# Optimization experiments

Measured on AMD Instinct MI355X. Metric: run time of the kernel, lower is better.

The kernel has to match this reference:

```python
import jax, jax.numpy as jnp
import numpy as np

N_NODE = 20000
N_EDGE = 200000
EMBED = 256
PAIR = 128
HEADS = 16
HEAD_DIM = EMBED // HEADS
SCALING = HEAD_DIM ** -0.5
EPS = 1e-5


def _ln(x, w, b):
    m = x.mean(-1, keepdims=True)
    v = ((x - m) ** 2).mean(-1, keepdims=True)
    return (x - m) / jnp.sqrt(v + EPS) * w + b


def setup_inputs() -> dict:
    key = jax.random.key(0)
    ks = jax.random.split(key, 12)
    inp = {
        "query": jax.random.normal(ks[0], (N_NODE, EMBED), jnp.float32),
        "edge_index": jax.random.randint(ks[1], (N_EDGE, 2), 0, N_NODE, jnp.int64 if jax.config.jax_enable_x64 else jnp.int32),
        "edge_diff": jax.random.normal(ks[2], (N_EDGE, 3), jnp.float32),
        "pair": jax.random.normal(ks[3], (N_EDGE, PAIR), jnp.float32),
        "ln_w": jnp.ones((EMBED,), jnp.float32),
        "ln_b": jnp.zeros((EMBED,), jnp.float32),
        "pln_w": jnp.ones((PAIR,), jnp.float32),
        "pln_b": jnp.zeros((PAIR,), jnp.float32),
        "Wq": jax.random.normal(ks[4], (EMBED, EMBED), jnp.float32) * 0.02,
        "Wk": jax.random.normal(ks[5], (EMBED, EMBED), jnp.float32) * 0.02,
        "Wv": jax.random.normal(ks[6], (EMBED, EMBED), jnp.float32) * 0.02,
        "Wb": jax.random.normal(ks[7], (HEADS, PAIR), jnp.float32) * 0.02,
        "bb": jnp.zeros((HEADS,), jnp.float32),
        "Wf1": jax.random.normal(ks[8], (1, EMBED), jnp.float32) * 0.02,
        "bf1": jnp.zeros((1,), jnp.float32),
        "Wf2": jax.random.normal(ks[9], (1, EMBED), jnp.float32) * 0.02,
        "bf2": jnp.zeros((1,), jnp.float32),
        "Wf3": jax.random.normal(ks[10], (1, EMBED), jnp.float32) * 0.02,
        "bf3": jnp.zeros((1,), jnp.float32),
    }
    return inp


def reference(query, edge_index, edge_diff, pair, ln_w, ln_b, pln_w, pln_b,
              Wq, Wk, Wv, Wb, bb, Wf1, bf1, Wf2, bf2, Wf3, bf3):
    n_node = query.shape[0]
    src = edge_index[:, 0]
    dst = edge_index[:, 1]

    qn = _ln(query, ln_w, ln_b)          # preln on node features
    pn = _ln(pair, pln_w, pln_b)         # preln on pair features

    q = (qn @ Wq.T).reshape(n_node, HEADS, HEAD_DIM)
    k = (qn @ Wk.T).reshape(n_node, HEADS, HEAD_DIM)
    v = (qn @ Wv.T).reshape(n_node, HEADS, HEAD_DIM)

    qe = q[src] * SCALING                # [E,H,D]
    ke = k[dst]
    ve = v[dst]

    logits = (qe * ke).sum(-1) + pn @ Wb.T + bb   # [E,H]

    # segment softmax over destination node (edge_index[:,0])
    seg_max = jax.ops.segment_max(logits, src, num_segments=n_node)  # [N,H]
    ex = jnp.exp(logits - seg_max[src])
    denom = jax.ops.segment_sum(ex, src, num_segments=n_node)
    probs = ex / denom[src]              # [E,H]

    # 3D-weighted scatter-sum: out[n,h,c,d] = sum_e probs[e,h]*diff[e,c]*v[e,h,d]
    w = probs[:, :, None] * edge_diff[:, None, :]                    # [E,H,3]
    contrib = w[:, :, :, None] * ve[:, :, None, :]                   # [E,H,3,D]
    x = jax.ops.segment_sum(contrib, src, num_segments=n_node)       # [N,H,3,D]
    x = x.transpose(0, 2, 1, 3).reshape(n_node, 3, EMBED)            # [N,3,H*D]

    f1 = x[:, 0, :] @ Wf1.T + bf1
    f2 = x[:, 1, :] @ Wf2.T + bf2
    f3 = x[:, 2, :] @ Wf3.T + bf3
    return jnp.concatenate([f1, f2, f3], axis=-1).astype(jnp.float32)
```

## Files before the change

### kernel.cpp

```cpp
#include <hip/hip_runtime.h>
#include <math.h>

#define N_NODE 20000
#define N_EDGE 200000
#define EMBED 256
#define PAIR 128
#define HEADS 16
#define HEAD_DIM 16
#define SCALING 0.25f
#define LNEPS 1e-5f

typedef unsigned short u16;
typedef unsigned int u32;
typedef __attribute__((ext_vector_type(8))) short bf16x8;
typedef __attribute__((ext_vector_type(4))) float f32x4;

#define WS_QKV   0
#define WS_QN    30720000
#define WS_WBF   40960000
#define WS_WW    41353216
#define WS_C0    41357312
#define WS_C1    41357376
#define WS_BIAS  41357440
#define WS_VW    54157440
#define WS_CNT   57997440
#define WS_CUR   58077440
#define WS_OFF   58157440
#define WS_REC   58237504

__device__ __forceinline__ u16 f2bf(float f) {
  u32 u = __float_as_uint(f);
  u32 r = (u + 0x7FFFu + ((u >> 16) & 1u)) >> 16;
  return (u16)r;
}
__device__ __forceinline__ float bl(u32 u) { return __uint_as_float(u << 16); }
__device__ __forceinline__ float bh(u32 u) { return __uint_as_float(u & 0xFFFF0000u); }

__device__ __forceinline__ float dot8(uint4 a, uint4 b) {
  float s = bl(a.x) * bl(b.x) + bh(a.x) * bh(b.x);
  s += bl(a.y) * bl(b.y) + bh(a.y) * bh(b.y);
  s += bl(a.z) * bl(b.z) + bh(a.z) * bh(b.z);
  s += bl(a.w) * bl(b.w) + bh(a.w) * bh(b.w);
  return s;
}

__global__ __launch_bounds__(256) void k1_pre_hist_kernel(
    const float* __restrict__ query, const float* __restrict__ ln_w,
    const float* __restrict__ ln_b, u16* __restrict__ qn,
    const float* __restrict__ Wq, const float* __restrict__ Wk,
    const float* __restrict__ Wv, u16* __restrict__ Wbf,
    const float* __restrict__ pln_w, const float* __restrict__ pln_b,
    const float* __restrict__ Wb, const float* __restrict__ bb,
    u16* __restrict__ WWbf, float* __restrict__ c0, float* __restrict__ c1,
    const int* __restrict__ edge_index, int* __restrict__ counts) {
  int bid = blockIdx.x;
  if (bid < 5000) {
    int node = bid * 4 + (threadIdx.x >> 6);
    int lane = threadIdx.x & 63;
    float4 a = *(const float4*)(query + (size_t)node * EMBED + lane * 4);
    float s = a.x + a.y + a.z + a.w;
    float s2 = a.x * a.x + a.y * a.y + a.z * a.z + a.w * a.w;
    #pragma unroll
    for (int off = 32; off > 0; off >>= 1) {
      s += __shfl_xor(s, off);
      s2 += __shfl_xor(s2, off);
    }
    float m = s * (1.0f / EMBED);
    float r = rsqrtf(s2 * (1.0f / EMBED) - m * m + LNEPS);
    float4 w4 = *(const float4*)(ln_w + lane * 4);
    float4 b4 = *(const float4*)(ln_b + lane * 4);
    ushort4 st;
    st.x = f2bf((a.x - m) * r * w4.x + b4.x);
    st.y = f2bf((a.y - m) * r * w4.y + b4.y);
    st.z = f2bf((a.z - m) * r * w4.z + b4.z);
    st.w = f2bf((a.w - m) * r * w4.w + b4.w);
    *(ushort4*)(qn + (size_t)node * EMBED + lane * 4) = st;
  } else if (bid < 5192) {
    int g4 = (bid - 5000) * 256 + threadIdx.x;
    int idx = g4 * 4;
    const float* src = (idx < 65536) ? Wq : (idx < 131072 ? Wk : Wv);
    float4 v = *(const float4*)(src + (idx & 65535));
    ushort4 st = {f2bf(v.x), f2bf(v.y), f2bf(v.z), f2bf(v.w)};
    *(ushort4*)(Wbf + idx) = st;
  } else if (bid == 5192) {
    if (threadIdx.x < 64) {
      int l = threadIdx.x;
      for (int h = 0; h < HEADS; h++) {
        int i0 = l * 2;
        float wb0 = Wb[h * PAIR + i0], wb1 = Wb[h * PAIR + i0 + 1];
        float ww0 = pln_w[i0] * wb0, ww1 = pln_w[i0 + 1] * wb1;
        WWbf[h * PAIR + i0] = f2bf(ww0);
        WWbf[h * PAIR + i0 + 1] = f2bf(ww1);
        float s1 = ww0 + ww1;
        float s0 = pln_b[i0] * wb0 + pln_b[i0 + 1] * wb1;
        #pragma unroll
        for (int off = 32; off > 0; off >>= 1) {
          s1 += __shfl_xor(s1, off);
          s0 += __shfl_xor(s0, off);
        }
        if (l == 0) {
          c1[h] = s1;
          c0[h] = s0 + bb[h];
        }
      }
    }
  } else {
    int e = (bid - 5193) * 256 + threadIdx.x;
    if (e < N_EDGE) atomicAdd(&counts[edge_index[e * 2]], 1);
  }
}

#define BKP 72
__global__ __launch_bounds__(256, 2) void k2_gemm_scan_kernel(
    const u16* __restrict__ qn, const u16* __restrict__ Wbf,
    u16* __restrict__ qkv, const int* __restrict__ counts,
    int* __restrict__ off) {
  int bid = blockIdx.x;
  int t = threadIdx.x;
  if (bid == 942) {
    __shared__ int part[256];
    int i0 = t * 79;
    int i1 = i0 + 79; if (i1 > N_NODE) i1 = N_NODE;
    int s = 0;
    for (int i = i0; i < i1; i++) s += counts[i];
    part[t] = s;
    __syncthreads();
    int x = s;
    for (int o = 1; o < 256; o <<= 1) {
      int y = (t >= o) ? part[t - o] : 0;
      __syncthreads();
      x += y;
      part[t] = x;
      __syncthreads();
    }
    int run = x - s;
    for (int i = i0; i < i1; i++) {
      off[i] = run;
      run += counts[i];
    }
    if (t == 255) off[N_NODE] = N_EDGE;
    return;
  }
  __shared__ u16 As[128 * BKP];
  __shared__ u16 Bs[128 * BKP];
  int bx = bid % 157, by = bid / 157;
  int wv = t >> 6, lane = t & 63;
  int quad = lane >> 4, l16 = lane & 15;
  int row0 = bx * 128, col0 = by * 128;
  int mt = (wv >> 1) * 64, nt = (wv & 1) * 64;

  f32x4 acc[4][4];
  #pragma unroll
  for (int im = 0; im < 4; im++)
    #pragma unroll
    for (int in_ = 0; in_ < 4; in_++) acc[im][in_] = (f32x4){0.f, 0.f, 0.f, 0.f};

  for (int it = 0; it < 4; it++) {
    int k0 = it * 64;
    #pragma unroll
    for (int j = 0; j < 4; j++) {
      int L = j * 256 + t;
      int row = L >> 3, slot = L & 7;
      int ra = min(row0 + row, N_NODE - 1);
      uint4 va = *(const uint4*)(qn + (size_t)ra * 256 + k0 + slot * 8);
      *(uint4*)(&As[row * BKP + slot * 8]) = va;
      uint4 vb = *(const uint4*)(Wbf + (size_t)(col0 + row) * 256 + k0 + slot * 8);
      *(uint4*)(&Bs[row * BKP + slot * 8]) = vb;
    }
    __syncthreads();
    #pragma unroll
    for (int s = 0; s < 2; s++) {
      int ko = s * 32 + quad * 8;
      bf16x8 af[4], bf[4];
      #pragma unroll
      for (int im = 0; im < 4; im++)
        af[im] = *(const bf16x8*)(&As[(mt + im * 16 + l16) * BKP + ko]);
      #pragma unroll
      for (int in_ = 0; in_ < 4; in_++)
        bf[in_] = *(const bf16x8*)(&Bs[(nt + in_ * 16 + l16) * BKP + ko]);
      #pragma unroll
      for (int im = 0; im < 4; im++)
        #pragma unroll
        for (int in_ = 0; in_ < 4; in_++)
          acc[im][in_] = __builtin_amdgcn_mfma_f32_16x16x32_bf16(
              af[im], bf[in_], acc[im][in_], 0, 0, 0);
    }
    __syncthreads();
  }
  #pragma unroll
  for (int im = 0; im < 4; im++) {
    #pragma unroll
    for (int in_ = 0; in_ < 4; in_++) {
      int gcol = col0 + nt + in_ * 16 + l16;
      float scale = (gcol < 256) ? SCALING : 1.0f;
      #pragma unroll
      for (int r = 0; r < 4; r++) {
        int grow = row0 + mt + im * 16 + quad * 4 + r;
        if (grow < N_NODE)
          qkv[(size_t)grow * 768 + gcol] = f2bf(acc[im][in_][r] * scale);
      }
    }
  }
}

#define PP 136
__global__ __launch_bounds__(256) void k3_bias_scatter_vw_kernel(
    const float* __restrict__ pair, const u16* __restrict__ WWbf,
    const float* __restrict__ c0g, const float* __restrict__ c1g,
    float* __restrict__ bias, const u16* __restrict__ qkv,
    const float* __restrict__ Wf1, const float* __restrict__ Wf2,
    const float* __restrict__ Wf3, float* __restrict__ vw,
    const int* __restrict__ edge_index, const float* __restrict__ edge_diff,
    const int* __restrict__ off, int* __restrict__ cur,
    uint4* __restrict__ rec) {
  int bid = blockIdx.x;
  int t = threadIdx.x;
  if (bid >= 3125) {
    int gid = (bid - 3125) * 256 + t;
    int n = gid >> 4, h = gid & 15;
    const uint4* vp = (const uint4*)(qkv + (size_t)n * 768 + 512 + h * 16);
    uint4 va = vp[0], vb = vp[1];
    float v[16];
    v[0] = bl(va.x); v[1] = bh(va.x); v[2] = bl(va.y); v[3] = bh(va.y);
    v[4] = bl(va.z); v[5] = bh(va.z); v[6] = bl(va.w); v[7] = bh(va.w);
    v[8] = bl(vb.x); v[9] = bh(vb.x); v[10] = bl(vb.y); v[11] = bh(vb.y);
    v[12] = bl(vb.z); v[13] = bh(vb.z); v[14] = bl(vb.w); v[15] = bh(vb.w);
    const float* wf[3] = {Wf1 + h * 16, Wf2 + h * 16, Wf3 + h * 16};
    #pragma unroll
    for (int c = 0; c < 3; c++) {
      float s = 0.f;
      #pragma unroll
      for (int d = 0; d < 16; d++) s += v[d] * wf[c][d];
      vw[(size_t)n * 48 + h * 3 + c] = s;
    }
    return;
  }
  __shared__ u16 Ps[64 * PP];
  __shared__ u16 WWs[16 * PP];
  __shared__ float ms[64], rs[64], c0s[16], c1s[16];
  __shared__ int pos_s[64];
  int wv = t >> 6, lane = t & 63;
  int quad = lane >> 4, l16 = lane & 15;
  int e0 = bid * 64;
  #pragma unroll
  for (int j = 0; j < 8; j++) {
    int L = j * 256 + t;
    int row = L >> 5, slot = L & 31;
    float4 p = *(const float4*)(pair + (size_t)(e0 + row) * PAIR + slot * 4);
    ushort4 st = {f2bf(p.x), f2bf(p.y), f2bf(p.z), f2bf(p.w)};
    *(ushort4*)(&Ps[row * PP + slot * 4]) = st;
  }
  #pragma unroll
  for (int j = 0; j < 2; j++) {
    int L = j * 256 + t;
    int row = L >> 5, slot = L & 31;
    ushort4 w = *(const ushort4*)(WWbf + row * PAIR + slot * 4);
    *(ushort4*)(&WWs[row * PP + slot * 4]) = w;
  }
  if (t < 16) {
    c0s[t] = c0g[t];
    c1s[t] = c1g[t];
  }
  if (t < 64) {
    int e = e0 + t;
    int srcn = edge_index[e * 2 + 0];
    int dstn = edge_index[e * 2 + 1];
    int pos = off[srcn] + atomicAdd(&cur[srcn], 1);
    pos_s[t] = pos;
    const float* dp = edge_diff + (size_t)e * 3;
    uint4 r;
    r.x = (u32)dstn;
    r.y = __float_as_uint(dp[0]);
    r.z = __float_as_uint(dp[1]);
    r.w = __float_as_uint(dp[2]);
    rec[pos] = r;
  }
  __syncthreads();
  {
    int row = t >> 2, qq = t & 3;
    float s = 0.f, s2 = 0.f;
    #pragma unroll
    for (int jj = 0; jj < 8; jj++) {
      ushort4 u = *(const ushort4*)(&Ps[row * PP + (qq * 8 + jj) * 4]);
      float x0 = __uint_as_float((u32)u.x << 16);
      float x1 = __uint_as_float((u32)u.y << 16);
      float x2 = __uint_as_float((u32)u.z << 16);
      float x3 = __uint_as_float((u32)u.w << 16);
      s += x0 + x1 + x2 + x3;
      s2 += x0 * x0 + x1 * x1 + x2 * x2 + x3 * x3;
    }
    s += __shfl_xor(s, 1); s += __shfl_xor(s, 2);
    s2 += __shfl_xor(s2, 1); s2 += __shfl_xor(s2, 2);
    if (qq == 0) {
      float m = s * (1.0f / PAIR);
      ms[row] = m;
      rs[row] = rsqrtf(s2 * (1.0f / PAIR) - m * m + LNEPS);
    }
  }
  __syncthreads();
  f32x4 acc = (f32x4){0.f, 0.f, 0.f, 0.f};
  #pragma unroll
  for (int sk = 0; sk < 4; sk++) {
    int ko = sk * 32 + quad * 8;
    bf16x8 a = *(const bf16x8*)(&Ps[(wv * 16 + l16) * PP + ko]);
    bf16x8 b = *(const bf16x8*)(&WWs[l16 * PP + ko]);
    acc = __builtin_amdgcn_mfma_f32_16x16x32_bf16(a, b, acc, 0, 0, 0);
  }
  #pragma unroll
  for (int r = 0; r < 4; r++) {
    int el = wv * 16 + quad * 4 + r;
    float bv = rs[el] * (acc[r] - ms[el] * c1s[l16]) + c0s[l16];
    bias[(size_t)pos_s[el] * HEADS + l16] = bv;
  }
}

__global__ __launch_bounds__(256) void seg_attn_kernel(
    const u16* __restrict__ qkv, const float* __restrict__ bias,
    const int* __restrict__ off, const uint4* __restrict__ rec,
    const float* __restrict__ vw, const float* __restrict__ bf1,
    const float* __restrict__ bf2, const float* __restrict__ bf3,
    float* __restrict__ out) {
  int wv = threadIdx.x >> 6, lane = threadIdx.x & 63;
  int src = blockIdx.x * 4 + wv;
  int h = lane & 15, eslot = lane >> 4;
  int lo = off[src];
  int deg = off[src + 1] - lo;
  const uint4* qp = (const uint4*)(qkv + (size_t)src * 768 + h * 16);
  uint4 q0 = qp[0], q1 = qp[1];
  float exsum = 0.f, a0 = 0.f, a1 = 0.f, a2 = 0.f;
  for (int ei = eslot; ei < deg; ei += 4) {
    uint4 rr = rec[lo + ei];
    int dst = (int)rr.x;
    float d0 = __uint_as_float(rr.y);
    float d1 = __uint_as_float(rr.z);
    float d2 = __uint_as_float(rr.w);
    const uint4* kp = (const uint4*)(qkv + (size_t)dst * 768 + 256 + h * 16);
    float d = dot8(q0, kp[0]) + dot8(q1, kp[1]);
    float ex = __expf(d + bias[(size_t)(lo + ei) * HEADS + h]);
    exsum += ex;
    const float* vp = vw + (size_t)dst * 48 + h * 3;
    a0 += ex * vp[0] * d0;
    a1 += ex * vp[1] * d1;
    a2 += ex * vp[2] * d2;
  }
  exsum += __shfl_xor(exsum, 16);
  exsum += __shfl_xor(exsum, 32);
  float rden = (exsum > 0.f) ? 1.0f / exsum : 0.f;
  a0 *= rden; a1 *= rden; a2 *= rden;
  #pragma unroll
  for (int o = 1; o < 64; o <<= 1) {
    a0 += __shfl_xor(a0, o);
    a1 += __shfl_xor(a1, o);
    a2 += __shfl_xor(a2, o);
  }
  if (lane == 0) {
    out[src * 3 + 0] = a0 + bf1[0];
    out[src * 3 + 1] = a1 + bf2[0];
    out[src * 3 + 2] = a2 + bf3[0];
  }
}

extern "C" void kernel_launch(void* const* d_in, const int* in_sizes, int n_in,
                              void* d_out, int out_size, void* d_ws,
                              size_t ws_size, hipStream_t stream) {
  const float* query      = (const float*)d_in[0];
  const int*   edge_index = (const int*)d_in[1];
  const float* edge_diff  = (const float*)d_in[2];
  const float* pair       = (const float*)d_in[3];
  const float* ln_w       = (const float*)d_in[4];
  const float* ln_b       = (const float*)d_in[5];
  const float* pln_w      = (const float*)d_in[6];
  const float* pln_b      = (const float*)d_in[7];
  const float* Wq         = (const float*)d_in[8];
  const float* Wk         = (const float*)d_in[9];
  const float* Wv         = (const float*)d_in[10];
  const float* Wb         = (const float*)d_in[11];
  const float* bb         = (const float*)d_in[12];
  const float* Wf1        = (const float*)d_in[13];
  const float* bf1        = (const float*)d_in[14];
  const float* Wf2        = (const float*)d_in[15];
  const float* bf2        = (const float*)d_in[16];
  const float* Wf3        = (const float*)d_in[17];
  const float* bf3        = (const float*)d_in[18];

  char* ws = (char*)d_ws;
  u16*   qkv   = (u16*)(ws + WS_QKV);
  u16*   qn    = (u16*)(ws + WS_QN);
  u16*   Wbf   = (u16*)(ws + WS_WBF);
  u16*   WWbf  = (u16*)(ws + WS_WW);
  float* c0    = (float*)(ws + WS_C0);
  float* c1    = (float*)(ws + WS_C1);
  float* bias  = (float*)(ws + WS_BIAS);
  float* vw    = (float*)(ws + WS_VW);
  int*   counts= (int*)(ws + WS_CNT);
  int*   cur   = (int*)(ws + WS_CUR);
  int*   off   = (int*)(ws + WS_OFF);
  uint4* rec   = (uint4*)(ws + WS_REC);
  float* out   = (float*)d_out;

  hipMemsetAsync(ws + WS_CNT, 0, 160000, stream);
  k1_pre_hist_kernel<<<5975, 256, 0, stream>>>(
      query, ln_w, ln_b, qn, Wq, Wk, Wv, Wbf, pln_w, pln_b, Wb, bb, WWbf, c0,
      c1, edge_index, counts);
  k2_gemm_scan_kernel<<<943, 256, 0, stream>>>(qn, Wbf, qkv, counts, off);
  k3_bias_scatter_vw_kernel<<<4375, 256, 0, stream>>>(
      pair, WWbf, c0, c1, bias, qkv, Wf1, Wf2, Wf3, vw, edge_index, edge_diff,
      off, cur, rec);
  seg_attn_kernel<<<N_NODE / 4, 256, 0, stream>>>(qkv, bias, off, rec, vw,
                                                  bf1, bf2, bf3, out);
}
```

Baseline: 305.3 us.

## Fold Wf projections into V weights and gather edge data by index

Precomputes combined weights Wv^T·Wf (48 rows, padded to 640) so the GEMM emits the per-node vw projection directly, dropping the full V output and the separate vw pass. The qkv buffer shrinks to 512 columns. The CSR scatter now stores only (dst, edge id) as int2 instead of a 16-byte record. Bias is written in edge order, and seg_attn gathers bias and edge_diff through the edge id. This cuts GEMM output traffic and scatter write volume, but it adds random gathers of bias and edge_diff in the attention loop and rounds the folded weights to bf16.

```diff
diff --git a/kernel.cpp b/kernel.cpp
--- a/kernel.cpp
+++ b/kernel.cpp
@@ -16,17 +16,17 @@
 typedef __attribute__((ext_vector_type(4))) float f32x4;
 
 #define WS_QKV   0
-#define WS_QN    30720000
-#define WS_WBF   40960000
-#define WS_WW    41353216
-#define WS_C0    41357312
-#define WS_C1    41357376
-#define WS_BIAS  41357440
-#define WS_VW    54157440
-#define WS_CNT   57997440
-#define WS_CUR   58077440
-#define WS_OFF   58157440
-#define WS_REC   58237504
+#define WS_QN    20480000
+#define WS_WBF   30720000
+#define WS_WW    31047680
+#define WS_C0    31051776
+#define WS_C1    31051840
+#define WS_BIAS  31051904
+#define WS_VW    43851904
+#define WS_CNT   47691904
+#define WS_CUR   47771904
+#define WS_OFF   47851904
+#define WS_DE    47931968
 
 __device__ __forceinline__ u16 f2bf(float f) {
   u32 u = __float_as_uint(f);
@@ -48,15 +48,18 @@
     const float* __restrict__ query, const float* __restrict__ ln_w,
     const float* __restrict__ ln_b, u16* __restrict__ qn,
     const float* __restrict__ Wq, const float* __restrict__ Wk,
-    const float* __restrict__ Wv, u16* __restrict__ Wbf,
+    const float* __restrict__ Wv, u16* __restrict__ WbfAll,
     const float* __restrict__ pln_w, const float* __restrict__ pln_b,
     const float* __restrict__ Wb, const float* __restrict__ bb,
     u16* __restrict__ WWbf, float* __restrict__ c0, float* __restrict__ c1,
-    const int* __restrict__ edge_index, int* __restrict__ counts) {
+    const float* __restrict__ Wf1, const float* __restrict__ Wf2,
+    const float* __restrict__ Wf3, const int* __restrict__ edge_index,
+    int* __restrict__ counts) {
   int bid = blockIdx.x;
+  int t = threadIdx.x;
   if (bid < 5000) {
-    int node = bid * 4 + (threadIdx.x >> 6);
-    int lane = threadIdx.x & 63;
+    int node = bid * 4 + (t >> 6);
+    int lane = t & 63;
     float4 a = *(const float4*)(query + (size_t)node * EMBED + lane * 4);
     float s = a.x + a.y + a.z + a.w;
     float s2 = a.x * a.x + a.y * a.y + a.z * a.z + a.w * a.w;
@@ -75,16 +78,16 @@
     st.z = f2bf((a.z - m) * r * w4.z + b4.z);
     st.w = f2bf((a.w - m) * r * w4.w + b4.w);
     *(ushort4*)(qn + (size_t)node * EMBED + lane * 4) = st;
-  } else if (bid < 5192) {
-    int g4 = (bid - 5000) * 256 + threadIdx.x;
+  } else if (bid < 5128) {
+    int g4 = (bid - 5000) * 256 + t;
     int idx = g4 * 4;
-    const float* src = (idx < 65536) ? Wq : (idx < 131072 ? Wk : Wv);
+    const float* src = (idx < 65536) ? Wq : Wk;
     float4 v = *(const float4*)(src + (idx & 65535));
     ushort4 st = {f2bf(v.x), f2bf(v.y), f2bf(v.z), f2bf(v.w)};
-    *(ushort4*)(Wbf + idx) = st;
-  } else if (bid == 5192) {
-    if (threadIdx.x < 64) {
-      int l = threadIdx.x;
+    *(ushort4*)(WbfAll + idx) = st;
+  } else if (bid == 5128) {
+    if (t < 64) {
+      int l = t;
       for (int h = 0; h < HEADS; h++) {
         int i0 = l * 2;
         float wb0 = Wb[h * PAIR + i0], wb1 = Wb[h * PAIR + i0 + 1];
@@ -104,20 +107,31 @@
         }
       }
     }
+  } else if (bid == 5129) {
+    for (int j = 0; j < 48; j++) {
+      int h = j / 3, c = j - h * 3;
+      const float* wf = (c == 0) ? Wf1 : ((c == 1) ? Wf2 : Wf3);
+      float s = 0.f;
+      #pragma unroll
+      for (int d = 0; d < 16; d++)
+        s += Wv[(size_t)(h * 16 + d) * 256 + t] * wf[h * 16 + d];
+      WbfAll[(size_t)(512 + j) * 256 + t] = f2bf(s);
+    }
+    for (int r = 0; r < 80; r++) WbfAll[(size_t)(560 + r) * 256 + t] = 0;
   } else {
-    int e = (bid - 5193) * 256 + threadIdx.x;
+    int e = (bid - 5130) * 256 + t;
     if (e < N_EDGE) atomicAdd(&counts[edge_index[e * 2]], 1);
   }
 }
 
 #define BKP 72
 __global__ __launch_bounds__(256, 2) void k2_gemm_scan_kernel(
-    const u16* __restrict__ qn, const u16* __restrict__ Wbf,
-    u16* __restrict__ qkv, const int* __restrict__ counts,
-    int* __restrict__ off) {
+    const u16* __restrict__ qn, const u16* __restrict__ WbfAll,
+    u16* __restrict__ qkv, float* __restrict__ vw,
+    const int* __restrict__ counts, int* __restrict__ off) {
   int bid = blockIdx.x;
   int t = threadIdx.x;
-  if (bid == 942) {
+  if (bid == 785) {
     __shared__ int part[256];
     int i0 = t * 79;
     int i1 = i0 + 79; if (i1 > N_NODE) i1 = N_NODE;
@@ -164,7 +178,7 @@
       int ra = min(row0 + row, N_NODE - 1);
       uint4 va = *(const uint4*)(qn + (size_t)ra * 256 + k0 + slot * 8);
       *(uint4*)(&As[row * BKP + slot * 8]) = va;
-      uint4 vb = *(const uint4*)(Wbf + (size_t)(col0 + row) * 256 + k0 + slot * 8);
+      uint4 vb = *(const uint4*)(WbfAll + (size_t)(col0 + row) * 256 + k0 + slot * 8);
       *(uint4*)(&Bs[row * BKP + slot * 8]) = vb;
     }
     __syncthreads();
@@ -196,49 +210,30 @@
       #pragma unroll
       for (int r = 0; r < 4; r++) {
         int grow = row0 + mt + im * 16 + quad * 4 + r;
-        if (grow < N_NODE)
-          qkv[(size_t)grow * 768 + gcol] = f2bf(acc[im][in_][r] * scale);
+        if (grow < N_NODE) {
+          if (gcol < 512) {
+            qkv[(size_t)grow * 512 + gcol] = f2bf(acc[im][in_][r] * scale);
+          } else if (gcol < 560) {
+            vw[(size_t)grow * 48 + (gcol - 512)] = acc[im][in_][r];
+          }
+        }
       }
     }
   }
 }
 
 #define PP 136
-__global__ __launch_bounds__(256) void k3_bias_scatter_vw_kernel(
+__global__ __launch_bounds__(256) void k3_bias_scatter_kernel(
     const float* __restrict__ pair, const u16* __restrict__ WWbf,
     const float* __restrict__ c0g, const float* __restrict__ c1g,
-    float* __restrict__ bias, const u16* __restrict__ qkv,
-    const float* __restrict__ Wf1, const float* __restrict__ Wf2,
-    const float* __restrict__ Wf3, float* __restrict__ vw,
-    const int* __restrict__ edge_index, const float* __restrict__ edge_diff,
+    float* __restrict__ bias, const int* __restrict__ edge_index,
     const int* __restrict__ off, int* __restrict__ cur,
-    uint4* __restrict__ rec) {
-  int bid = blockIdx.x;
-  int t = threadIdx.x;
-  if (bid >= 3125) {
-    int gid = (bid - 3125) * 256 + t;
-    int n = gid >> 4, h = gid & 15;
-    const uint4* vp = (const uint4*)(qkv + (size_t)n * 768 + 512 + h * 16);
-    uint4 va = vp[0], vb = vp[1];
-    float v[16];
-    v[0] = bl(va.x); v[1] = bh(va.x); v[2] = bl(va.y); v[3] = bh(va.y);
-    v[4] = bl(va.z); v[5] = bh(va.z); v[6] = bl(va.w); v[7] = bh(va.w);
-    v[8] = bl(vb.x); v[9] = bh(vb.x); v[10] = bl(vb.y); v[11] = bh(vb.y);
-    v[12] = bl(vb.z); v[13] = bh(vb.z); v[14] = bl(vb.w); v[15] = bh(vb.w);
-    const float* wf[3] = {Wf1 + h * 16, Wf2 + h * 16, Wf3 + h * 16};
-    #pragma unroll
-    for (int c = 0; c < 3; c++) {
-      float s = 0.f;
-      #pragma unroll
-      for (int d = 0; d < 16; d++) s += v[d] * wf[c][d];
-      vw[(size_t)n * 48 + h * 3 + c] = s;
-    }
-    return;
-  }
+    int2* __restrict__ de) {
   __shared__ u16 Ps[64 * PP];
   __shared__ u16 WWs[16 * PP];
   __shared__ float ms[64], rs[64], c0s[16], c1s[16];
-  __shared__ int pos_s[64];
+  int bid = blockIdx.x;
+  int t = threadIdx.x;
   int wv = t >> 6, lane = t & 63;
   int quad = lane >> 4, l16 = lane & 15;
   int e0 = bid * 64;
@@ -266,14 +261,7 @@
     int srcn = edge_index[e * 2 + 0];
     int dstn = edge_index[e * 2 + 1];
     int pos = off[srcn] + atomicAdd(&cur[srcn], 1);
-    pos_s[t] = pos;
-    const float* dp = edge_diff + (size_t)e * 3;
-    uint4 r;
-    r.x = (u32)dstn;
-    r.y = __float_as_uint(dp[0]);
-    r.z = __float_as_uint(dp[1]);
-    r.w = __float_as_uint(dp[2]);
-    rec[pos] = r;
+    de[pos] = make_int2(dstn, e);
   }
   __syncthreads();
   {
@@ -310,38 +298,35 @@
   for (int r = 0; r < 4; r++) {
     int el = wv * 16 + quad * 4 + r;
     float bv = rs[el] * (acc[r] - ms[el] * c1s[l16]) + c0s[l16];
-    bias[(size_t)pos_s[el] * HEADS + l16] = bv;
+    bias[(size_t)(e0 + el) * HEADS + l16] = bv;
   }
 }
 
 __global__ __launch_bounds__(256) void seg_attn_kernel(
     const u16* __restrict__ qkv, const float* __restrict__ bias,
-    const int* __restrict__ off, const uint4* __restrict__ rec,
-    const float* __restrict__ vw, const float* __restrict__ bf1,
-    const float* __restrict__ bf2, const float* __restrict__ bf3,
-    float* __restrict__ out) {
+    const int* __restrict__ off, const int2* __restrict__ de,
+    const float* __restrict__ vw, const float* __restrict__ edge_diff,
+    const float* __restrict__ bf1, const float* __restrict__ bf2,
+    const float* __restrict__ bf3, float* __restrict__ out) {
   int wv = threadIdx.x >> 6, lane = threadIdx.x & 63;
   int src = blockIdx.x * 4 + wv;
   int h = lane & 15, eslot = lane >> 4;
   int lo = off[src];
   int deg = off[src + 1] - lo;
-  const uint4* qp = (const uint4*)(qkv + (size_t)src * 768 + h * 16);
+  const uint4* qp = (const uint4*)(qkv + (size_t)src * 512 + h * 16);
   uint4 q0 = qp[0], q1 = qp[1];
   float exsum = 0.f, a0 = 0.f, a1 = 0.f, a2 = 0.f;
   for (int ei = eslot; ei < deg; ei += 4) {
-    uint4 rr = rec[lo + ei];
-    int dst = (int)rr.x;
-    float d0 = __uint_as_float(rr.y);
-    float d1 = __uint_as_float(rr.z);
-    float d2 = __uint_as_float(rr.w);
-    const uint4* kp = (const uint4*)(qkv + (size_t)dst * 768 + 256 + h * 16);
+    int2 d_e = de[lo + ei];
+    const uint4* kp = (const uint4*)(qkv + (size_t)d_e.x * 512 + 256 + h * 16);
     float d = dot8(q0, kp[0]) + dot8(q1, kp[1]);
-    float ex = __expf(d + bias[(size_t)(lo + ei) * HEADS + h]);
+    float ex = __expf(d + bias[(size_t)d_e.y * HEADS + h]);
     exsum += ex;
-    const float* vp = vw + (size_t)dst * 48 + h * 3;
-    a0 += ex * vp[0] * d0;
-    a1 += ex * vp[1] * d1;
-    a2 += ex * vp[2] * d2;
+    const float* vp = vw + (size_t)d_e.x * 48 + h * 3;
+    const float* dp = edge_diff + (size_t)d_e.y * 3;
+    a0 += ex * vp[0] * dp[0];
+    a1 += ex * vp[1] * dp[1];
+    a2 += ex * vp[2] * dp[2];
   }
   exsum += __shfl_xor(exsum, 16);
   exsum += __shfl_xor(exsum, 32);
@@ -386,7 +371,7 @@
   char* ws = (char*)d_ws;
   u16*   qkv   = (u16*)(ws + WS_QKV);
   u16*   qn    = (u16*)(ws + WS_QN);
-  u16*   Wbf   = (u16*)(ws + WS_WBF);
+  u16*   WbfAll= (u16*)(ws + WS_WBF);
   u16*   WWbf  = (u16*)(ws + WS_WW);
   float* c0    = (float*)(ws + WS_C0);
   float* c1    = (float*)(ws + WS_C1);
@@ -395,17 +380,18 @@
   int*   counts= (int*)(ws + WS_CNT);
   int*   cur   = (int*)(ws + WS_CUR);
   int*   off   = (int*)(ws + WS_OFF);
-  uint4* rec   = (uint4*)(ws + WS_REC);
+  int2*  de    = (int2*)(ws + WS_DE);
   float* out   = (float*)d_out;
 
   hipMemsetAsync(ws + WS_CNT, 0, 160000, stream);
-  k1_pre_hist_kernel<<<5975, 256, 0, stream>>>(
-      query, ln_w, ln_b, qn, Wq, Wk, Wv, Wbf, pln_w, pln_b, Wb, bb, WWbf, c0,
-      c1, edge_index, counts);
-  k2_gemm_scan_kernel<<<943, 256, 0, stream>>>(qn, Wbf, qkv, counts, off);
-  k3_bias_scatter_vw_kernel<<<4375, 256, 0, stream>>>(
-      pair, WWbf, c0, c1, bias, qkv, Wf1, Wf2, Wf3, vw, edge_index, edge_diff,
-      off, cur, rec);
-  seg_attn_kernel<<<N_NODE / 4, 256, 0, stream>>>(qkv, bias, off, rec, vw,
-                                                  bf1, bf2, bf3, out);
-}
+  k1_pre_hist_kernel<<<5912, 256, 0, stream>>>(
+      query, ln_w, ln_b, qn, Wq, Wk, Wv, WbfAll, pln_w, pln_b, Wb, bb, WWbf,
+      c0, c1, Wf1, Wf2, Wf3, edge_index, counts);
+  k2_gemm_scan_kernel<<<786, 256, 0, stream>>>(qn, WbfAll, qkv, vw, counts,
+                                               off);
+  k3_bias_scatter_kernel<<<3125, 256, 0, stream>>>(
+      pair, WWbf, c0, c1, bias, edge_index, off, cur, de);
+  seg_attn_kernel<<<N_NODE / 4, 256, 0, stream>>>(qkv, bias, off, de, vw,
+                                                  edge_diff, bf1, bf2, bf3,
+                                                  out);
+}
```

New measurement: 317.6 us. 1.04x slower.
